# Kernel tuning notes

Measured on AMD Instinct MI355X. Metric: run time of the kernel, lower is better.

Reference implementation:

```python
import jax, jax.numpy as jnp
import numpy as np

N_FFT = 2048
HOP = 512


def setup_inputs() -> dict:
    key = jax.random.key(0)
    x = jax.random.normal(key, (16, 1048576), dtype=jnp.float32)
    return {"x": x}


def reference(x):
    # causal buffer: fresh module state -> zeros of shape [..., frames_out*hop]
    frames_out = N_FFT // HOP - 1  # 3
    buf = jnp.zeros(x.shape[:-1] + (frames_out * HOP,), dtype=x.dtype)
    xc = jnp.concatenate([buf, x], axis=-1)  # [B, T + 1536]
    L = xc.shape[-1]
    num_frames = (L - N_FFT) // HOP + 1
    # strided framing via gather: out[..., f, t] = xc[..., f*hop + t]
    idx = jnp.arange(num_frames)[:, None] * HOP + jnp.arange(N_FFT)[None, :]
    return xc[..., idx]  # [B, num_frames, n_fft]
```

## Files before the change

### kernel.cpp

```cpp
#include <hip/hip_runtime.h>
#include <hip/hip_bf16.h>


#define B_DIM   16
#define T_LEN   1048576u
#define N_FFT   2048
#define HOP     512
#define PREFIX  1536
#define NFRAMES 2048

__global__ __launch_bounds__(256) void frame_kernel(
    const float* __restrict__ x, float4* __restrict__ out)
{
    unsigned int gid = blockIdx.x * blockDim.x + threadIdx.x;
    unsigned int t4 = gid & 511u;
    unsigned int f  = (gid >> 9) & 2047u;
    unsigned int b  = gid >> 20;

    int i = (int)(f * HOP + t4 * 4u);
    float4 v;
    if (i >= PREFIX) {
        v = *reinterpret_cast<const float4*>(
                x + (size_t)b * T_LEN + (unsigned)(i - PREFIX));
    } else {
        v = make_float4(0.f, 0.f, 0.f, 0.f);
    }
    out[gid] = v;
}

extern "C" void kernel_launch(void* const* d_in, const int* in_sizes, int n_in,
                              void* d_out, int out_size, void* d_ws, size_t ws_size,
                              hipStream_t stream) {
    const float* x = (const float*)d_in[0];
    float4* out = (float4*)d_out;
    const unsigned int n4 = 16u * 2048u * 2048u / 4u;
    dim3 block(256);
    dim3 grid(n4 / 256u);
    frame_kernel<<<grid, block, 0, stream>>>(x, out);
}
```

Measured before the change: 77.84 us.

## Invert framing to scatter each input chunk to its overlapping frames

```diff
diff --git a/kernel.cpp b/kernel.cpp
--- a/kernel.cpp
+++ b/kernel.cpp
@@ -2,39 +2,48 @@
 #include <hip/hip_bf16.h>
 
 
-#define B_DIM   16
-#define T_LEN   1048576u
-#define N_FFT   2048
-#define HOP     512
-#define PREFIX  1536
-#define NFRAMES 2048
+#define T4_PER_B   262144u
+#define R4         128u
+#define QI_COUNT   2051u
+#define NFRAMES    2048u
 
-__global__ __launch_bounds__(256) void frame_kernel(
-    const float* __restrict__ x, float4* __restrict__ out)
+__global__ __launch_bounds__(256) void scatter_frames(
+    const float4* __restrict__ x4, float4* __restrict__ out4)
 {
     unsigned int gid = blockIdx.x * blockDim.x + threadIdx.x;
-    unsigned int t4 = gid & 511u;
-    unsigned int f  = (gid >> 9) & 2047u;
-    unsigned int b  = gid >> 20;
+    const unsigned int total = 16u * QI_COUNT * R4;
+    if (gid >= total) return;
 
-    int i = (int)(f * HOP + t4 * 4u);
+    unsigned int r4 = gid & (R4 - 1u);
+    unsigned int rest = gid >> 7;
+    unsigned int qi = rest % QI_COUNT;
+    unsigned int b  = rest / QI_COUNT;
+    int q = (int)qi - 3;
+
     float4 v;
-    if (i >= PREFIX) {
-        v = *reinterpret_cast<const float4*>(
-                x + (size_t)b * T_LEN + (unsigned)(i - PREFIX));
+    if (q >= 0) {
+        v = x4[(size_t)b * T4_PER_B + (unsigned)q * R4 + r4];
     } else {
         v = make_float4(0.f, 0.f, 0.f, 0.f);
     }
-    out[gid] = v;
+
+    size_t obase = ((size_t)b * NFRAMES) * 512u + r4;
+#pragma unroll
+    for (int k = 0; k < 4; ++k) {
+        int f = q + k;
+        if (f >= 0 && f < (int)NFRAMES) {
+            out4[obase + (size_t)f * 512u + (unsigned)(3 - k) * 128u] = v;
+        }
+    }
 }
 
 extern "C" void kernel_launch(void* const* d_in, const int* in_sizes, int n_in,
                               void* d_out, int out_size, void* d_ws, size_t ws_size,
                               hipStream_t stream) {
-    const float* x = (const float*)d_in[0];
-    float4* out = (float4*)d_out;
-    const unsigned int n4 = 16u * 2048u * 2048u / 4u;
+    const float4* x4 = (const float4*)d_in[0];
+    float4* out4 = (float4*)d_out;
+    const unsigned int total = 16u * QI_COUNT * R4;
     dim3 block(256);
-    dim3 grid(n4 / 256u);
-    frame_kernel<<<grid, block, 0, stream>>>(x, out);
+    dim3 grid((total + 255u) / 256u);
+    scatter_frames<<<grid, block, 0, stream>>>(x4, out4);
 }
```

Measured after the change: 66.05 us. -15.2%, faster.
